# Kernel optimization log

Measured on AMD Instinct MI355X. Metric: run time of the kernel, lower is better.

## Reference

```python
import jax, jax.numpy as jnp
import numpy as np

B, T, D, H = 4, 2048, 1024, 16
HD = D // H


def setup_inputs() -> dict:
    key = jax.random.key(0)
    ks = jax.random.split(key, 9)
    s = 1.0 / np.sqrt(D)
    return {
        "x": jax.random.normal(ks[0], (B, T, D), dtype=jnp.float32),
        "Wq": jax.random.normal(ks[1], (D, D), dtype=jnp.float32) * s,
        "bq": jnp.zeros((D,), dtype=jnp.float32),
        "Wk": jax.random.normal(ks[2], (D, D), dtype=jnp.float32) * s,
        "bk": jnp.zeros((D,), dtype=jnp.float32),
        "Wv": jax.random.normal(ks[3], (D, D), dtype=jnp.float32) * s,
        "bv": jnp.zeros((D,), dtype=jnp.float32),
        "Wo": jax.random.normal(ks[4], (D, D), dtype=jnp.float32) * s,
        "bo": jnp.zeros((D,), dtype=jnp.float32),
    }


def reference(x, Wq, bq, Wk, bk, Wv, bv, Wo, bo):
    b, t, c = x.shape
    h, hd = H, HD
    scale = hd ** -0.5
    # projections: [B,T,C] -> [B,H,T,hd]
    q = (x @ Wq.T + bq).reshape(b, t, h, hd).transpose(0, 2, 1, 3)
    k = (x @ Wk.T + bk).reshape(b, t, h, hd).transpose(0, 2, 1, 3)
    v = (x @ Wv.T + bv).reshape(b, t, h, hd).transpose(0, 2, 1, 3)
    # scores [B,H,T,T], causal mask (no kv cache path, T > 1)
    attn = jnp.einsum("bhqd,bhkd->bhqk", q, k) * scale
    causal = jnp.triu(jnp.ones((t, t), dtype=bool), k=1)
    attn = jnp.where(causal, -jnp.inf, attn)
    attn = jax.nn.softmax(attn, axis=-1)
    out = jnp.einsum("bhqk,bhkd->bhqd", attn, v)
    out = out.transpose(0, 2, 1, 3).reshape(b, t, c)
    return (out @ Wo.T + bo, k, v)
```

## Files before the change

### kernel.cpp

```cpp
#include <hip/hip_runtime.h>
#include <hip/hip_bf16.h>
#include <cstdint>


typedef short bf16x8 __attribute__((ext_vector_type(8)));
typedef float f32x4 __attribute__((ext_vector_type(4)));

#define GLDS16(g, l)                                                          \
  __builtin_amdgcn_global_load_lds(                                           \
      (const __attribute__((address_space(1))) void*)(g),                     \
      (__attribute__((address_space(3))) void*)(l), 16, 0, 0)

static __device__ __forceinline__ short f2b(float f) {
  union { float f; unsigned u; } x; x.f = f;
  unsigned r = (x.u + 0x7FFFu + ((x.u >> 16) & 1u)) >> 16;
  return (short)r;
}

static __device__ __forceinline__ unsigned cvtpk2(float a, float b) {
  unsigned r;
  asm("v_cvt_pk_bf16_f32 %0, %1, %2" : "=v"(r) : "v"(a), "v"(b));
  return r;
}

__global__ void cvt_all(const float* __restrict__ x,
                        const float* __restrict__ a, const float* __restrict__ b,
                        const float* __restrict__ c, const float* __restrict__ d,
                        short* __restrict__ xb, short* __restrict__ wb) {
  int i = blockIdx.x * blockDim.x + threadIdx.x;
  if (i < 2097152) {
    float4 v = ((const float4*)x)[i];
    short4 o; o.x = f2b(v.x); o.y = f2b(v.y); o.z = f2b(v.z); o.w = f2b(v.w);
    ((short4*)xb)[i] = o;
  } else {
    int k = i - 2097152;
    int sel = k >> 18;
    const float* src = sel == 0 ? a : sel == 1 ? b : sel == 2 ? c : d;
    int off = k & 262143;
    float4 v = ((const float4*)src)[off];
    short4 o; o.x = f2b(v.x); o.y = f2b(v.y); o.z = f2b(v.z); o.w = f2b(v.w);
    ((short4*)wb)[k] = o;
  }
}

#define PIPE_STEP(BUF)                                                        \
  {                                                                          \
    asm volatile("s_waitcnt vmcnt(4) lgkmcnt(0)" ::: "memory");              \
    __builtin_amdgcn_s_barrier();                                            \
    __builtin_amdgcn_sched_barrier(0);                                       \
    stage((((BUF) + 2) % 3), (tile + 2) * 32);                               \
    compute(BUF);                                                            \
    ++tile;                                                                  \
  }

#define PIPE_TAIL()                                                          \
  asm volatile("s_waitcnt vmcnt(4) lgkmcnt(0)" ::: "memory");                \
  __builtin_amdgcn_s_barrier();                                              \
  __builtin_amdgcn_sched_barrier(0);                                         \
  compute(0);                                                   \
  asm volatile("s_waitcnt vmcnt(0) lgkmcnt(0)" ::: "memory");                \
  __builtin_amdgcn_s_barrier();                                              \
  __builtin_amdgcn_sched_barrier(0);                                         \
  compute(1);

__global__ __launch_bounds__(256) void gemm_qkv(
    const short* __restrict__ A,
    const short* __restrict__ W0, const short* __restrict__ W1, const short* __restrict__ W2,
    const float* __restrict__ b0, const float* __restrict__ b1, const float* __restrict__ b2,
    float* __restrict__ kf, float* __restrict__ vf,
    short* __restrict__ qbo, short* __restrict__ kbo, short* __restrict__ vtbo) {
  __shared__ short SM[24576];
  const int t = threadIdx.x;
  const int lane = t & 63;
  const int w = t >> 6;
  const int wm = w >> 1, wn = w & 1;
  const int quad = lane >> 4, l15 = lane & 15;
  const int bm = blockIdx.y;
  const int sel = blockIdx.x >> 3, bn = blockIdx.x & 7;
  const short* Bm = sel == 0 ? W0 : (sel == 1 ? W1 : W2);
  const float* bias = sel == 0 ? b0 : (sel == 1 ? b1 : b2);

  f32x4 acc[4][4];
  for (int i = 0; i < 4; i++)
    for (int j = 0; j < 4; j++) acc[i][j] = (f32x4){0.f, 0.f, 0.f, 0.f};

  const int c0 = t, c1 = t + 256;
  const int r0 = c0 >> 2, cc0 = c0 & 3;
  const int r1 = c1 >> 2, cc1 = c1 & 3;
  const short* Abase = A + (size_t)bm * 128 * 1024;
  const short* Bbase = Bm + (size_t)bn * 128 * 1024;

  auto stage = [&](int buf, int kk) {
    short* A_ = SM + buf * 4096;
    short* B_ = SM + 12288 + buf * 4096;
    GLDS16(Abase + (size_t)r0 * 1024 + kk + cc0 * 8, A_ + c0 * 8);
    GLDS16(Abase + (size_t)r1 * 1024 + kk + cc1 * 8, A_ + c1 * 8);
    GLDS16(Bbase + (size_t)r0 * 1024 + kk + cc0 * 8, B_ + c0 * 8);
    GLDS16(Bbase + (size_t)r1 * 1024 + kk + cc1 * 8, B_ + c1 * 8);
  };
  auto compute = [&](int buf) {
    const short* A_ = SM + buf * 4096;
    const short* B_ = SM + 12288 + buf * 4096;
    bf16x8 af[4], bfr[4];
    for (int mt = 0; mt < 4; mt++)
      af[mt] = *(const bf16x8*)(A_ + (wm * 64 + mt * 16 + l15) * 32 + quad * 8);
    for (int nt = 0; nt < 4; nt++)
      bfr[nt] = *(const bf16x8*)(B_ + (wn * 64 + nt * 16 + l15) * 32 + quad * 8);
    for (int mt = 0; mt < 4; mt++)
      for (int nt = 0; nt < 4; nt++)
        acc[mt][nt] = __builtin_amdgcn_mfma_f32_16x16x32_bf16(af[mt], bfr[nt], acc[mt][nt], 0, 0, 0);
  };

  stage(0, 0);
  stage(1, 32);
  int tile = 0;
  for (int ii = 0; ii < 10; ++ii) {
    PIPE_STEP(0) PIPE_STEP(1) PIPE_STEP(2)
  }
  PIPE_TAIL()

  if (sel != 2) {
    for (int mt = 0; mt < 4; mt++) {
      const int row_base = bm * 128 + wm * 64 + mt * 16 + quad * 4;
      for (int nt = 0; nt < 4; nt++) {
        const int col = bn * 128 + wn * 64 + nt * 16 + l15;
        const float bb = bias[col];
        for (int r = 0; r < 4; r++) {
          const int row = row_base + r;
          const float v = acc[mt][nt][r] + bb;
          const int b = row >> 11, tt = row & 2047;
          const int h = col >> 6, hi = col & 63;
          const size_t idx = (((size_t)(b * 16 + h)) * 2048 + tt) * 64 + hi;
          if (sel == 0) {
            qbo[idx] = f2b(v);
          } else {
            kf[idx] = v; kbo[idx] = f2b(v);
          }
        }
      }
    }
  } else {
    short* Tr = SM;
    __syncthreads();
    for (int mt = 0; mt < 4; mt++) {
      const int rowb = wm * 64 + mt * 16 + quad * 4;
      const int growb = bm * 128 + rowb;
      const int b_ = growb >> 11;
      for (int nt = 0; nt < 4; nt++) {
        const int colL = wn * 64 + nt * 16 + l15;
        const int col = bn * 128 + colL;
        const float bb = bias[col];
        const int h_ = col >> 6, hi_ = col & 63;
        short4 pk;
        for (int r = 0; r < 4; r++) {
          const float v = acc[mt][nt][r] + bb;
          const int tt = (growb + r) & 2047;
          vf[(((size_t)(b_ * 16 + h_)) * 2048 + tt) * 64 + hi_] = v;
          ((short*)&pk)[r] = f2b(v);
        }
        *(short4*)&Tr[colL * 136 + rowb] = pk;
      }
    }
    __syncthreads();
    const int c = t & 127, half = t >> 7;
    const int gcol = bn * 128 + c;
    const int h_ = gcol >> 6, hi_ = gcol & 63;
    for (int j = 0; j < 8; j++) {
      const int chunk = half * 8 + j;
      const int row0 = bm * 128 + chunk * 8;
      const int b_ = row0 >> 11, tt = row0 & 2047;
      bf16x8 val = *(const bf16x8*)&Tr[c * 136 + chunk * 8];
      *(bf16x8*)&vtbo[(((size_t)(b_ * 16 + h_)) * 64 + hi_) * 2048 + tt] = val;
    }
  }
}

__global__ __launch_bounds__(256) void gemm_o(
    const short* __restrict__ A, const short* __restrict__ Bm,
    const float* __restrict__ bias, float* __restrict__ out_f) {
  __shared__ short SM[24576];
  const int t = threadIdx.x;
  const int lane = t & 63;
  const int w = t >> 6;
  const int wm = w >> 1, wn = w & 1;
  const int quad = lane >> 4, l15 = lane & 15;
  const int bm = blockIdx.y, bn = blockIdx.x;

  f32x4 acc[4][4];
  for (int i = 0; i < 4; i++)
    for (int j = 0; j < 4; j++) acc[i][j] = (f32x4){0.f, 0.f, 0.f, 0.f};

  const int c0 = t, c1 = t + 256;
  const int r0 = c0 >> 2, cc0 = c0 & 3;
  const int r1 = c1 >> 2, cc1 = c1 & 3;
  const short* Abase = A + (size_t)bm * 128 * 1024;
  const short* Bbase = Bm + (size_t)bn * 128 * 1024;

  auto stage = [&](int buf, int kk) {
    short* A_ = SM + buf * 4096;
    short* B_ = SM + 12288 + buf * 4096;
    GLDS16(Abase + (size_t)r0 * 1024 + kk + cc0 * 8, A_ + c0 * 8);
    GLDS16(Abase + (size_t)r1 * 1024 + kk + cc1 * 8, A_ + c1 * 8);
    GLDS16(Bbase + (size_t)r0 * 1024 + kk + cc0 * 8, B_ + c0 * 8);
    GLDS16(Bbase + (size_t)r1 * 1024 + kk + cc1 * 8, B_ + c1 * 8);
  };
  auto compute = [&](int buf) {
    const short* A_ = SM + buf * 4096;
    const short* B_ = SM + 12288 + buf * 4096;
    bf16x8 af[4], bfr[4];
    for (int mt = 0; mt < 4; mt++)
      af[mt] = *(const bf16x8*)(A_ + (wm * 64 + mt * 16 + l15) * 32 + quad * 8);
    for (int nt = 0; nt < 4; nt++)
      bfr[nt] = *(const bf16x8*)(B_ + (wn * 64 + nt * 16 + l15) * 32 + quad * 8);
    for (int mt = 0; mt < 4; mt++)
      for (int nt = 0; nt < 4; nt++)
        acc[mt][nt] = __builtin_amdgcn_mfma_f32_16x16x32_bf16(af[mt], bfr[nt], acc[mt][nt], 0, 0, 0);
  };

  stage(0, 0);
  stage(1, 32);
  int tile = 0;
  for (int ii = 0; ii < 10; ++ii) {
    PIPE_STEP(0) PIPE_STEP(1) PIPE_STEP(2)
  }
  PIPE_TAIL()

  for (int mt = 0; mt < 4; mt++) {
    const int row_base = bm * 128 + wm * 64 + mt * 16 + quad * 4;
    for (int nt = 0; nt < 4; nt++) {
      const int col = bn * 128 + wn * 64 + nt * 16 + l15;
      const float bb = bias[col];
      for (int r = 0; r < 4; r++) {
        const int row = row_base + r;
        out_f[(size_t)row * 1024 + col] = acc[mt][nt][r] + bb;
      }
    }
  }
}

__global__ __launch_bounds__(256, 4) void attn_fwd(
    const short* __restrict__ Qb, const short* __restrict__ Kb,
    const short* __restrict__ VTb, short* __restrict__ Ob) {
  __shared__ short Ks[128 * 64];
  __shared__ short VTs[64 * 128];
  const int t = threadIdx.x;
  const int w = t >> 6;
  const int lane = t & 63;
  const int quad = lane >> 4, l15 = lane & 15;

  const int L = blockIdx.x + (blockIdx.y << 4);
  const int work = ((L & 7) << 7) + (L >> 3);
  const int bh = work >> 4;
  const int base = work & 15;
  const int b = bh >> 4, h = bh & 15;

  const short* Qh = Qb + (size_t)bh * 2048 * 64;
  const short* Kh = Kb + (size_t)bh * 2048 * 64;
  const short* VTh = VTb + (size_t)bh * 64 * 2048;
  unsigned* Pd = (unsigned*)Ks + w * 1024;
  const int swz = (l15 & 7) << 2;
  const float sscale = 0.125f * 1.4426950408889634f;

  for (int s = 0; s < 2; ++s) {
    const int qt = s ? (31 - base) : base;
    const int q0 = qt * 64 + w * 16;
    const bf16x8 qf0 = *(const bf16x8*)(Qh + (q0 + l15) * 64 + quad * 8);
    const bf16x8 qf1 = *(const bf16x8*)(Qh + (q0 + l15) * 64 + quad * 8 + 32);

    float m_q = -1e30f, l_q = 0.f;
    f32x4 o[4];
    for (int nt = 0; nt < 4; nt++) o[nt] = (f32x4){0.f, 0.f, 0.f, 0.f};
    const int ntile = (qt >> 1) + 1;

    for (int jt = 0; jt < ntile; ++jt) {
      const int j0 = jt << 7;
      __syncthreads();
      for (int rr = 0; rr < 4; rr++) {
        const int c = rr * 256 + t;
        const int row = c >> 3, colL = c & 7;
        const int colg = colL ^ (row & 7);
        GLDS16(Kh + (size_t)(j0 + row) * 64 + colg * 8, &Ks[c * 8]);
      }
      for (int rr = 0; rr < 4; rr++) {
        const int c = rr * 256 + t;
        const int row = c >> 4, colL = c & 15;
        const int colg = colL ^ (row & 7);
        GLDS16(VTh + (size_t)row * 2048 + j0 + colg * 8, &VTs[c * 8]);
      }
      __syncthreads();

      float sv[8][4];
      for (int si = 0; si < 8; ++si) {
        const int r = si * 16 + l15;
        bf16x8 kf0 = *(const bf16x8*)&Ks[(r * 8 + (quad ^ (r & 7))) * 8];
        bf16x8 kf1 = *(const bf16x8*)&Ks[(r * 8 + ((quad ^ 4) ^ (r & 7))) * 8];
        f32x4 z = (f32x4){0.f, 0.f, 0.f, 0.f};
        z = __builtin_amdgcn_mfma_f32_16x16x32_bf16(kf0, qf0, z, 0, 0, 0);
        z = __builtin_amdgcn_mfma_f32_16x16x32_bf16(kf1, qf1, z, 0, 0, 0);
        for (int r4 = 0; r4 < 4; r4++) sv[si][r4] = z[r4];
      }
      if (jt == ntile - 1) {
        const int qg = q0 + l15;
        for (int si = 0; si < 8; si++) {
          const int kbase = j0 + si * 16 + quad * 4;
          for (int r4 = 0; r4 < 4; r4++)
            if (kbase + r4 > qg) sv[si][r4] = -1e30f;
        }
      }
      float vmax = fmaxf(fmaxf(sv[0][0], sv[0][1]), fmaxf(sv[0][2], sv[0][3]));
      for (int si = 1; si < 8; si++) {
        float m2 = fmaxf(fmaxf(sv[si][0], sv[si][1]), fmaxf(sv[si][2], sv[si][3]));
        vmax = fmaxf(vmax, m2);
      }
      vmax = fmaxf(vmax, __shfl_xor(vmax, 16));
      vmax = fmaxf(vmax, __shfl_xor(vmax, 32));
      const float mn = fmaxf(m_q, vmax);
      if (__any(vmax > m_q)) {
        const float alpha = __builtin_amdgcn_exp2f((m_q - mn) * sscale);
        l_q *= alpha;
        float ar[4];
        for (int r4 = 0; r4 < 4; r4++) ar[r4] = __shfl(alpha, quad * 4 + r4);
        for (int nt = 0; nt < 4; nt++)
          for (int r4 = 0; r4 < 4; r4++) o[nt][r4] *= ar[r4];
      }
      m_q = mn;
      __syncthreads();

      const float negmns = -mn * sscale;
      float ssum = 0.f;
      for (int si = 0; si < 8; si++) {
        float p0 = __builtin_amdgcn_exp2f(fmaf(sv[si][0], sscale, negmns));
        float p1 = __builtin_amdgcn_exp2f(fmaf(sv[si][1], sscale, negmns));
        float p2 = __builtin_amdgcn_exp2f(fmaf(sv[si][2], sscale, negmns));
        float p3 = __builtin_amdgcn_exp2f(fmaf(sv[si][3], sscale, negmns));
        ssum += (p0 + p1) + (p2 + p3);
        uint2 pk; pk.x = cvtpk2(p0, p1); pk.y = cvtpk2(p2, p3);
        *(uint2*)(Pd + l15 * 64 + ((si * 8 + quad * 2) ^ swz)) = pk;
      }
      ssum += __shfl_xor(ssum, 16);
      ssum += __shfl_xor(ssum, 32);
      l_q += ssum;

      for (int kc = 0; kc < 4; kc++) {
        bf16x8 pf = *(const bf16x8*)(Pd + l15 * 64 + ((kc * 16 + quad * 4) ^ swz));
        for (int nt = 0; nt < 4; nt++) {
          const int rv = nt * 16 + l15;
          bf16x8 vf = *(const bf16x8*)&VTs[(rv * 16 + ((kc * 4 + quad) ^ (rv & 7))) * 8];
          o[nt] = __builtin_amdgcn_mfma_f32_16x16x32_bf16(pf, vf, o[nt], 0, 0, 0);
        }
      }
    }

    float lr[4], ri[4];
    for (int r4 = 0; r4 < 4; r4++) lr[r4] = __shfl(l_q, quad * 4 + r4);
    for (int r4 = 0; r4 < 4; r4++) ri[r4] = __builtin_amdgcn_rcpf(lr[r4]);
    for (int nt = 0; nt < 4; nt++) {
      const int col = h * 64 + nt * 16 + l15;
      for (int r4 = 0; r4 < 4; r4++) {
        const int q = q0 + quad * 4 + r4;
        Ob[((size_t)b * 2048 + q) * 1024 + col] = f2b(o[nt][r4] * ri[r4]);
      }
    }
  }
}

extern "C" void kernel_launch(void* const* d_in, const int* in_sizes, int n_in,
                              void* d_out, int out_size, void* d_ws, size_t ws_size,
                              hipStream_t stream) {
  const float* x  = (const float*)d_in[0];
  const float* Wq = (const float*)d_in[1];
  const float* bq = (const float*)d_in[2];
  const float* Wk = (const float*)d_in[3];
  const float* bk = (const float*)d_in[4];
  const float* Wv = (const float*)d_in[5];
  const float* bv = (const float*)d_in[6];
  const float* Wo = (const float*)d_in[7];
  const float* bo = (const float*)d_in[8];

  float* out   = (float*)d_out;
  float* k_out = out + (size_t)8388608;
  float* v_out = out + (size_t)16777216;

  short* ws  = (short*)d_ws;
  short* xb   = ws;
  short* wqb  = ws + 8388608;
  short* wkb  = ws + 9437184;
  short* wvb  = ws + 10485760;
  short* wob  = ws + 11534336;
  short* qb   = ws + 12582912;
  short* kb   = ws + 20971520;
  short* vtb  = ws + 29360128;
  short* attb = ws + 37748736;

  cvt_all<<<12288, 256, 0, stream>>>(x, Wq, Wk, Wv, Wo, xb, wqb);

  gemm_qkv<<<dim3(24, 64), 256, 0, stream>>>(
      xb, wqb, wkb, wvb, bq, bk, bv, k_out, v_out, qb, kb, vtb);

  attn_fwd<<<dim3(16, 64), 256, 0, stream>>>(qb, kb, vtb, attb);

  gemm_o<<<dim3(8, 64), 256, 0, stream>>>(attb, wob, bo, out);
}
```

Baseline: 326.0 us.

## Register-prefetch next K/V tile to overlap global loads with attention compute

```diff
diff --git a/kernel.cpp b/kernel.cpp
--- a/kernel.cpp
+++ b/kernel.cpp
@@ -10,6 +10,19 @@
   __builtin_amdgcn_global_load_lds(                                           \
       (const __attribute__((address_space(1))) void*)(g),                     \
       (__attribute__((address_space(3))) void*)(l), 16, 0, 0)
+
+#define LDS_FENCE()                                                           \
+  do {                                                                        \
+    asm volatile("s_waitcnt lgkmcnt(0)" ::: "memory");                        \
+    __builtin_amdgcn_sched_barrier(0);                                        \
+  } while (0)
+
+#define LGKM_BARRIER()                                                        \
+  do {                                                                        \
+    asm volatile("s_waitcnt lgkmcnt(0)" ::: "memory");                        \
+    __builtin_amdgcn_s_barrier();                                             \
+    __builtin_amdgcn_sched_barrier(0);                                        \
+  } while (0)
 
 static __device__ __forceinline__ short f2b(float f) {
   union { float f; unsigned u; } x; x.f = f;
@@ -261,6 +274,32 @@
   const int swz = (l15 & 7) << 2;
   const float sscale = 0.125f * 1.4426950408889634f;
 
+  bf16x8 pk_[4], pv_[4];
+  auto prefetch = [&](int j0) {
+    for (int rr = 0; rr < 4; rr++) {
+      const int c = rr * 256 + t;
+      const int row = c >> 3, colL = c & 7;
+      const int colg = colL ^ (row & 7);
+      pk_[rr] = *(const bf16x8*)(Kh + (size_t)(j0 + row) * 64 + colg * 8);
+    }
+    for (int rr = 0; rr < 4; rr++) {
+      const int c = rr * 256 + t;
+      const int row = c >> 4, colL = c & 15;
+      const int colg = colL ^ (row & 7);
+      pv_[rr] = *(const bf16x8*)(VTh + (size_t)row * 2048 + j0 + colg * 8);
+    }
+  };
+  auto store_lds = [&]() {
+    for (int rr = 0; rr < 4; rr++) {
+      const int c = rr * 256 + t;
+      *(bf16x8*)&Ks[c * 8] = pk_[rr];
+    }
+    for (int rr = 0; rr < 4; rr++) {
+      const int c = rr * 256 + t;
+      *(bf16x8*)&VTs[c * 8] = pv_[rr];
+    }
+  };
+
   for (int s = 0; s < 2; ++s) {
     const int qt = s ? (31 - base) : base;
     const int q0 = qt * 64 + w * 16;
@@ -272,22 +311,13 @@
     for (int nt = 0; nt < 4; nt++) o[nt] = (f32x4){0.f, 0.f, 0.f, 0.f};
     const int ntile = (qt >> 1) + 1;
 
+    prefetch(0);
     for (int jt = 0; jt < ntile; ++jt) {
       const int j0 = jt << 7;
       __syncthreads();
-      for (int rr = 0; rr < 4; rr++) {
-        const int c = rr * 256 + t;
-        const int row = c >> 3, colL = c & 7;
-        const int colg = colL ^ (row & 7);
-        GLDS16(Kh + (size_t)(j0 + row) * 64 + colg * 8, &Ks[c * 8]);
-      }
-      for (int rr = 0; rr < 4; rr++) {
-        const int c = rr * 256 + t;
-        const int row = c >> 4, colL = c & 15;
-        const int colg = colL ^ (row & 7);
-        GLDS16(VTh + (size_t)row * 2048 + j0 + colg * 8, &VTs[c * 8]);
-      }
+      store_lds();
       __syncthreads();
+      if (jt + 1 < ntile) prefetch(j0 + 128);
 
       float sv[8][4];
       for (int si = 0; si < 8; ++si) {
@@ -324,7 +354,7 @@
           for (int r4 = 0; r4 < 4; r4++) o[nt][r4] *= ar[r4];
       }
       m_q = mn;
-      __syncthreads();
+      LGKM_BARRIER();
 
       const float negmns = -mn * sscale;
       float ssum = 0.f;
@@ -340,6 +370,7 @@
       ssum += __shfl_xor(ssum, 16);
       ssum += __shfl_xor(ssum, 32);
       l_q += ssum;
+      LDS_FENCE();
 
       for (int kc = 0; kc < 4; kc++) {
         bf16x8 pf = *(const bf16x8*)(Pd + l15 * 64 + ((kc * 16 + quad * 4) ^ swz));
```

After: 423.4 us. +29.9%, slower.
